# Performance work log

Measured on AMD Instinct MI355X. Metric: run time of the kernel, lower is better.

## Reference

```python
import jax, jax.numpy as jnp
import numpy as np

B = 16384
F = 26          # num categorical fields
V = 100000      # vocab per field (equal sizes)
N = 13          # num numeric fields
D = 32          # embed_dim
HIDDEN = [256, 128, 64]


def setup_inputs() -> dict:
    key = jax.random.key(0)
    ks = jax.random.split(key, 16)
    x_cat = jax.random.randint(ks[0], (B, F), 0, V)
    x_num = jax.random.normal(ks[1], (B, N), dtype=jnp.float32)
    # first-order and second-order embedding tables (all fields stacked)
    emb0 = jax.random.normal(ks[2], (F, V), dtype=jnp.float32) * 0.01      # linear weights per cat value
    emb1 = jax.random.normal(ks[3], (F, V, D), dtype=jnp.float32) * 0.01   # latent vectors per cat value
    num_bias = jnp.zeros((N,), dtype=jnp.float32)
    num_emb = jax.random.normal(ks[4], (N, D), dtype=jnp.float32) * 0.01
    # MLP params: input_dim = (F+N)*D -> 256 -> 128 -> 64
    dims = [(F + N) * D] + HIDDEN
    params = {}
    for i in range(len(HIDDEN)):
        fan_in = dims[i]
        bound = 1.0 / np.sqrt(fan_in)
        params[f"W{i+1}"] = jax.random.uniform(ks[5 + 2 * i], (fan_in, dims[i + 1]), minval=-bound, maxval=bound, dtype=jnp.float32)
        params[f"b{i+1}"] = jax.random.uniform(ks[6 + 2 * i], (dims[i + 1],), minval=-bound, maxval=bound, dtype=jnp.float32)
    head_in = HIDDEN[-1] + 2
    hb = 1.0 / np.sqrt(head_in)
    Wc = jax.random.uniform(ks[11], (head_in, 1), minval=-hb, maxval=hb, dtype=jnp.float32)
    bc = jax.random.uniform(ks[12], (1,), minval=-hb, maxval=hb, dtype=jnp.float32)
    Wo = jax.random.uniform(ks[13], (head_in, 1), minval=-hb, maxval=hb, dtype=jnp.float32)
    bo = jax.random.uniform(ks[14], (1,), minval=-hb, maxval=hb, dtype=jnp.float32)
    return {"x_cat": x_cat, "x_num": x_num, "emb0": emb0, "emb1": emb1,
            "num_bias": num_bias, "num_emb": num_emb,
            "W1": params["W1"], "b1": params["b1"],
            "W2": params["W2"], "b2": params["b2"],
            "W3": params["W3"], "b3": params["b3"],
            "Wc": Wc, "bc": bc, "Wo": Wo, "bo": bo}


def reference(x_cat, x_num, emb0, emb1, num_bias, num_emb,
              W1, b1, W2, b2, W3, b3, Wc, bc, Wo, bo):
    f_idx = jnp.arange(F)
    # ---- first-order (linear) term ----
    linear_cat = emb0[f_idx[None, :], x_cat]                 # [B, F]
    linear_num = x_num * num_bias[None, :]                   # [B, N]
    linear_term = (linear_cat.sum(axis=1) + linear_num.sum(axis=1))[:, None]  # [B, 1]
    # ---- embeddings for FM + deep ----
    cat_e = emb1[f_idx[None, :], x_cat]                      # [B, F, D] fused gather
    num_e = x_num[:, :, None] * num_emb[None, :, :]          # [B, N, D]
    all_emb = jnp.concatenate([cat_e, num_e], axis=1)        # [B, F+N, D]
    # ---- FM second-order: 0.5 * sum((sum v)^2 - sum v^2) ----
    sum_emb = all_emb.sum(axis=1)                            # [B, D]
    square_sum = (all_emb * all_emb).sum(axis=1)             # [B, D]
    fm_second = 0.5 * (sum_emb * sum_emb - square_sum).sum(axis=1, keepdims=True)  # [B, 1]
    # ---- deep MLP (dropout = identity in eval) ----
    h = all_emb.reshape(all_emb.shape[0], -1)                # [B, (F+N)*D]
    h = jax.nn.relu(h @ W1 + b1)
    h = jax.nn.relu(h @ W2 + b2)
    h = jax.nn.relu(h @ W3 + b3)
    concat = jnp.concatenate([h, linear_term, fm_second], axis=1)  # [B, 66]
    logit1 = concat @ Wc + bc
    logit2 = concat @ Wo + bo
    return logit1, logit2
```

## Files before the change

### kernel.cpp

```cpp
#include <hip/hip_runtime.h>
#include <stdint.h>

#define B_ROWS 16384
#define NF 26
#define NV 100000
#define NN 13
#define ND 32
#define K1DIM 1248
#define H1DIM 256
#define H2DIM 128
#define H3DIM 64

typedef float f32x4 __attribute__((ext_vector_type(4)));
typedef short bf16x8 __attribute__((ext_vector_type(8)));

static __device__ __forceinline__ unsigned short f2bf(float f) {
    unsigned int u = __float_as_uint(f);
    unsigned int r = (u + 0x7fffu + ((u >> 16) & 1u)) >> 16;
    return (unsigned short)r;
}

static __device__ __forceinline__ void store_bf4(unsigned short* p, f32x4 e) {
    uint2 u;
    u.x = (unsigned)f2bf(e.x) | ((unsigned)f2bf(e.y) << 16);
    u.y = (unsigned)f2bf(e.z) | ((unsigned)f2bf(e.w) << 16);
    *(uint2*)p = u;
}

#define S1P ((K1DIM/32)*H1DIM*32)
#define S2P ((H1DIM/32)*H2DIM*32)
#define S3P ((H2DIM/32)*H3DIM*32)
#define EMB_BLOCKS 512
#define RPK_BLOCKS ((S1P + S2P + S3P) / 256)

__global__ __launch_bounds__(256) void prep(
    const int* __restrict__ x_cat, const float* __restrict__ x_num,
    const float* __restrict__ emb0, const float* __restrict__ emb1,
    const float* __restrict__ num_bias, const float* __restrict__ num_emb,
    const float* __restrict__ W1, const float* __restrict__ W2, const float* __restrict__ W3,
    unsigned short* __restrict__ Xp, float* __restrict__ lin_out, float* __restrict__ fm_out,
    unsigned short* __restrict__ W1p, unsigned short* __restrict__ W2p, unsigned short* __restrict__ W3p)
{
    if (blockIdx.x >= EMB_BLOCKS) {
        int tid = (blockIdx.x - EMB_BLOCKS) * 256 + threadIdx.x;
        if (tid < S1P) {
            int kk = tid & 31; int n = (tid >> 5) & (H1DIM - 1); int kt = tid >> 13;
            W1p[tid] = f2bf(W1[(kt * 32 + kk) * H1DIM + n]);
        } else if (tid < S1P + S2P) {
            int t = tid - S1P;
            int kk = t & 31; int n = (t >> 5) & (H2DIM - 1); int kt = t >> 12;
            W2p[t] = f2bf(W2[(kt * 32 + kk) * H2DIM + n]);
        } else {
            int t = tid - S1P - S2P;
            int kk = t & 31; int n = (t >> 5) & (H3DIM - 1); int kt = t >> 11;
            W3p[t] = f2bf(W3[(kt * 32 + kk) * H3DIM + n]);
        }
        return;
    }

    int sub = threadIdx.x & 7;
    int row = blockIdx.x * 32 + (threadIdx.x >> 3);
    int lanebase = (threadIdx.x & 63) & 56;

    const int* xc = x_cat + row * NF;
    int idxh[4];
#pragma unroll
    for (int j = 0; j < 4; j++) { int f = sub + 8 * j; idxh[j] = (f < NF) ? xc[f] : 0; }
    float numh[2];
    numh[0] = x_num[row * NN + sub];
    numh[1] = (sub < NN - 8) ? x_num[row * NN + sub + 8] : 0.f;

    float lv = 0.f;
#pragma unroll
    for (int j = 0; j < 4; j++) { int f = sub + 8 * j; if (f < NF) lv += emb0[f * NV + idxh[j]]; }
    lv += numh[0] * num_bias[sub];
    if (sub < NN - 8) lv += numh[1] * num_bias[sub + 8];

    unsigned short* xr = Xp + (size_t)row * K1DIM;
    f32x4 s4 = (f32x4){0.f, 0.f, 0.f, 0.f};
    f32x4 q4 = (f32x4){0.f, 0.f, 0.f, 0.f};

#pragma unroll
    for (int f = 0; f < NF; ++f) {
        int idx = __shfl(idxh[f >> 3], lanebase + (f & 7), 64);
        f32x4 e = ((const f32x4*)(emb1 + (size_t)(f * NV + idx) * ND))[sub];
        s4 += e; q4 += e * e;
        store_bf4(xr + f * ND + sub * 4, e);
    }
#pragma unroll
    for (int n = 0; n < NN; ++n) {
        float xv = __shfl(numh[n >> 3], lanebase + (n & 7), 64);
        f32x4 w = ((const f32x4*)(num_emb + n * ND))[sub];
        f32x4 e = w * xv;
        s4 += e; q4 += e * e;
        store_bf4(xr + (NF + n) * ND + sub * 4, e);
    }

    float val = s4.x * s4.x + s4.y * s4.y + s4.z * s4.z + s4.w * s4.w
              - (q4.x + q4.y + q4.z + q4.w);
#pragma unroll
    for (int m = 1; m < 8; m <<= 1) {
        val += __shfl_xor(val, m, 64);
        lv  += __shfl_xor(lv,  m, 64);
    }
    if (sub == 0) { fm_out[row] = 0.5f * val; lin_out[row] = lv; }
}

template<int TMM, int TMN>
__global__ __launch_bounds__(256) void gemm_relu(
    const unsigned short* __restrict__ X, const unsigned short* __restrict__ Wp,
    const float* __restrict__ bias, unsigned short* __restrict__ Y,
    int M, int N, int K)
{
    int wave = blockIdx.x * 4 + (threadIdx.x >> 6);
    int lane = threadIdx.x & 63;
    int l15 = lane & 15, quad = lane >> 4;
    int nWaveN = N / (16 * TMN);
    int wm = wave / nWaveN, wn = wave % nWaveN;
    int m0 = wm * 16 * TMM, n0 = wn * 16 * TMN;

    f32x4 acc[TMM][TMN];
#pragma unroll
    for (int i = 0; i < TMM; i++)
#pragma unroll
        for (int j = 0; j < TMN; j++) acc[i][j] = (f32x4){0.f, 0.f, 0.f, 0.f};

    const unsigned short* aptr = X + (size_t)(m0 + l15) * K + quad * 8;
    const unsigned short* bptr = Wp + ((size_t)n0 + l15) * 32 + quad * 8;
    const int KT = K >> 5;

    bf16x8 a[TMM], b[TMN];
#pragma unroll
    for (int i = 0; i < TMM; i++) a[i] = *(const bf16x8*)(aptr + (size_t)i * 16 * K);
#pragma unroll
    for (int j = 0; j < TMN; j++) b[j] = *(const bf16x8*)(bptr + (size_t)j * 16 * 32);

    for (int kt = 0; kt < KT - 1; ++kt) {
        bf16x8 an[TMM], bn[TMN];
        const unsigned short* ap = aptr + (size_t)(kt + 1) * 32;
        const unsigned short* bp = bptr + (size_t)(kt + 1) * N * 32;
#pragma unroll
        for (int i = 0; i < TMM; i++) an[i] = *(const bf16x8*)(ap + (size_t)i * 16 * K);
#pragma unroll
        for (int j = 0; j < TMN; j++) bn[j] = *(const bf16x8*)(bp + (size_t)j * 16 * 32);
#pragma unroll
        for (int i = 0; i < TMM; i++)
#pragma unroll
            for (int j = 0; j < TMN; j++)
                acc[i][j] = __builtin_amdgcn_mfma_f32_16x16x32_bf16(a[i], b[j], acc[i][j], 0, 0, 0);
#pragma unroll
        for (int i = 0; i < TMM; i++) a[i] = an[i];
#pragma unroll
        for (int j = 0; j < TMN; j++) b[j] = bn[j];
    }
#pragma unroll
    for (int i = 0; i < TMM; i++)
#pragma unroll
        for (int j = 0; j < TMN; j++)
            acc[i][j] = __builtin_amdgcn_mfma_f32_16x16x32_bf16(a[i], b[j], acc[i][j], 0, 0, 0);

#pragma unroll
    for (int j = 0; j < TMN; j++) {
        int col = n0 + j * 16 + l15;
        float bv = bias[col];
#pragma unroll
        for (int i = 0; i < TMM; i++) {
            int rbase = m0 + i * 16 + quad * 4;
#pragma unroll
            for (int r = 0; r < 4; r++) {
                float v = acc[i][j][r] + bv;
                v = v > 0.f ? v : 0.f;
                Y[(size_t)(rbase + r) * N + col] = f2bf(v);
            }
        }
    }
}

#define LDP 136
__global__ __launch_bounds__(256) void gemm23_head(
    const unsigned short* __restrict__ H1, const unsigned short* __restrict__ W2p,
    const float* __restrict__ b2,
    const unsigned short* __restrict__ W3p, const float* __restrict__ b3,
    const float* __restrict__ Wc, const float* __restrict__ bc,
    const float* __restrict__ Wo, const float* __restrict__ bo,
    const float* __restrict__ lin, const float* __restrict__ fm,
    float* __restrict__ out)
{
    __shared__ unsigned short lds[4 * 16 * LDP];
    int wid  = threadIdx.x >> 6;
    int wave = blockIdx.x * 4 + wid;
    int lane = threadIdx.x & 63;
    int l15 = lane & 15, quad = lane >> 4;
    int m0 = wave * 16;
    unsigned short* wlds = lds + wid * 16 * LDP;

    f32x4 acc2[8];
#pragma unroll
    for (int j = 0; j < 8; j++) acc2[j] = (f32x4){0.f, 0.f, 0.f, 0.f};

    const unsigned short* aptr = H1 + (size_t)(m0 + l15) * H1DIM + quad * 8;
    const unsigned short* bptr = W2p + l15 * 32 + quad * 8;
#pragma unroll
    for (int kt = 0; kt < 8; ++kt) {
        bf16x8 a = *(const bf16x8*)(aptr + kt * 32);
#pragma unroll
        for (int j = 0; j < 8; j++) {
            bf16x8 b = *(const bf16x8*)(bptr + (kt * H2DIM + j * 16) * 32);
            acc2[j] = __builtin_amdgcn_mfma_f32_16x16x32_bf16(a, b, acc2[j], 0, 0, 0);
        }
    }
#pragma unroll
    for (int j = 0; j < 8; j++) {
        int col = j * 16 + l15;
        float bv = b2[col];
#pragma unroll
        for (int r = 0; r < 4; r++) {
            float v = acc2[j][r] + bv;
            v = v > 0.f ? v : 0.f;
            wlds[(quad * 4 + r) * LDP + col] = f2bf(v);
        }
    }
    __syncthreads();

    f32x4 acc3[4];
#pragma unroll
    for (int j = 0; j < 4; j++) acc3[j] = (f32x4){0.f, 0.f, 0.f, 0.f};

    const unsigned short* b3ptr = W3p + l15 * 32 + quad * 8;
#pragma unroll
    for (int kt = 0; kt < 4; ++kt) {
        bf16x8 a = *(const bf16x8*)(wlds + l15 * LDP + kt * 32 + quad * 8);
#pragma unroll
        for (int j = 0; j < 4; j++) {
            bf16x8 b = *(const bf16x8*)(b3ptr + (kt * H3DIM + j * 16) * 32);
            acc3[j] = __builtin_amdgcn_mfma_f32_16x16x32_bf16(a, b, acc3[j], 0, 0, 0);
        }
    }

    float s1r[4] = {0.f, 0.f, 0.f, 0.f};
    float s2r[4] = {0.f, 0.f, 0.f, 0.f};
#pragma unroll
    for (int j = 0; j < 4; j++) {
        int col = j * 16 + l15;
        float bv = b3[col], wc = Wc[col], wo = Wo[col];
#pragma unroll
        for (int r = 0; r < 4; r++) {
            float v = acc3[j][r] + bv;
            v = v > 0.f ? v : 0.f;
            s1r[r] += v * wc;
            s2r[r] += v * wo;
        }
    }
#pragma unroll
    for (int r = 0; r < 4; r++) {
#pragma unroll
        for (int m = 8; m >= 1; m >>= 1) {
            s1r[r] += __shfl_xor(s1r[r], m, 16);
            s2r[r] += __shfl_xor(s2r[r], m, 16);
        }
    }
    if (l15 == 0) {
        float wc64 = Wc[64], wc65 = Wc[65], wo64 = Wo[64], wo65 = Wo[65];
        float bcv = bc[0], bov = bo[0];
#pragma unroll
        for (int r = 0; r < 4; r++) {
            int row = m0 + quad * 4 + r;
            float lt = lin[row], f2 = fm[row];
            out[row]          = s1r[r] + lt * wc64 + f2 * wc65 + bcv;
            out[B_ROWS + row] = s2r[r] + lt * wo64 + f2 * wo65 + bov;
        }
    }
}

#define OFF_XP   ((size_t)0)
#define OFF_W1P  ((size_t)40894464)
#define OFF_W2P  (OFF_W1P + 638976)
#define OFF_W3P  (OFF_W2P + 65536)
#define OFF_H1   (OFF_W3P + 16384)
#define OFF_LIN  (OFF_H1 + 8388608)
#define OFF_FM   (OFF_LIN + 65536)

extern "C" void kernel_launch(void* const* d_in, const int* in_sizes, int n_in,
                              void* d_out, int out_size, void* d_ws, size_t ws_size,
                              hipStream_t stream)
{
    const int*   x_cat    = (const int*)d_in[0];
    const float* x_num    = (const float*)d_in[1];
    const float* emb0     = (const float*)d_in[2];
    const float* emb1     = (const float*)d_in[3];
    const float* num_bias = (const float*)d_in[4];
    const float* num_emb  = (const float*)d_in[5];
    const float* W1 = (const float*)d_in[6];
    const float* b1 = (const float*)d_in[7];
    const float* W2 = (const float*)d_in[8];
    const float* b2 = (const float*)d_in[9];
    const float* W3 = (const float*)d_in[10];
    const float* b3 = (const float*)d_in[11];
    const float* Wc = (const float*)d_in[12];
    const float* bc = (const float*)d_in[13];
    const float* Wo = (const float*)d_in[14];
    const float* bo = (const float*)d_in[15];
    float* out = (float*)d_out;

    char* ws = (char*)d_ws;
    unsigned short* Xp  = (unsigned short*)(ws + OFF_XP);
    unsigned short* W1p = (unsigned short*)(ws + OFF_W1P);
    unsigned short* W2p = (unsigned short*)(ws + OFF_W2P);
    unsigned short* W3p = (unsigned short*)(ws + OFF_W3P);
    unsigned short* H1  = (unsigned short*)(ws + OFF_H1);
    float* lin = (float*)(ws + OFF_LIN);
    float* fm  = (float*)(ws + OFF_FM);

    prep<<<EMB_BLOCKS + RPK_BLOCKS, 256, 0, stream>>>(
        x_cat, x_num, emb0, emb1, num_bias, num_emb, W1, W2, W3,
        Xp, lin, fm, W1p, W2p, W3p);
    gemm_relu<2, 2><<<1024, 256, 0, stream>>>(Xp, W1p, b1, H1, B_ROWS, H1DIM, K1DIM);
    gemm23_head<<<B_ROWS / 16 / 4, 256, 0, stream>>>(H1, W2p, b2, W3p, b3, Wc, bc, Wo, bo, lin, fm, out);
}
```

Measured before the change: 466.6 us.

## Fuse embedding gather, three MLP layers and head into one LDS-resident kernel

Replaces the separate embedding/prep, layer-1 GEMM and layer-2/3/head kernels with one fused kernel. Each 32-row block gathers its embeddings straight into shared memory, then runs all three GEMMs and the heads from LDS. Weight repacking moves to its own small kernel. This removes the global round-trip of the 40MB bf16 activation matrix and the H1 buffer, at the cost of large LDS use (about 80KB per block), which limits occupancy. Every block also re-streams all of W1 from cache, with only 512 blocks of 32 rows each.

```diff
diff --git a/kernel.cpp b/kernel.cpp
--- a/kernel.cpp
+++ b/kernel.cpp
@@ -11,6 +11,11 @@
 #define H2DIM 128
 #define H3DIM 64
 
+#define XSTR  1256
+#define H1STR 264
+#define H2STR 136
+#define H2OFF (32 * H1STR)
+
 typedef float f32x4 __attribute__((ext_vector_type(4)));
 typedef short bf16x8 __attribute__((ext_vector_type(8)));
 
@@ -20,265 +25,257 @@
     return (unsigned short)r;
 }
 
-static __device__ __forceinline__ void store_bf4(unsigned short* p, f32x4 e) {
+static __device__ __forceinline__ uint2 pack_bf4(f32x4 e) {
     uint2 u;
     u.x = (unsigned)f2bf(e.x) | ((unsigned)f2bf(e.y) << 16);
     u.y = (unsigned)f2bf(e.z) | ((unsigned)f2bf(e.w) << 16);
-    *(uint2*)p = u;
+    return u;
 }
 
 #define S1P ((K1DIM/32)*H1DIM*32)
 #define S2P ((H1DIM/32)*H2DIM*32)
 #define S3P ((H2DIM/32)*H3DIM*32)
-#define EMB_BLOCKS 512
-#define RPK_BLOCKS ((S1P + S2P + S3P) / 256)
-
-__global__ __launch_bounds__(256) void prep(
+
+__global__ __launch_bounds__(256) void repack_weights(
+    const float* __restrict__ W1, const float* __restrict__ W2, const float* __restrict__ W3,
+    unsigned short* __restrict__ W1p, unsigned short* __restrict__ W2p, unsigned short* __restrict__ W3p)
+{
+    int tid = blockIdx.x * 256 + threadIdx.x;
+    if (tid < S1P) {
+        int kk = tid & 31; int n = (tid >> 5) & (H1DIM - 1); int kt = tid >> 13;
+        W1p[tid] = f2bf(W1[(kt * 32 + kk) * H1DIM + n]);
+    } else if (tid < S1P + S2P) {
+        int t = tid - S1P;
+        int kk = t & 31; int n = (t >> 5) & (H2DIM - 1); int kt = t >> 12;
+        W2p[t] = f2bf(W2[(kt * 32 + kk) * H2DIM + n]);
+    } else if (tid < S1P + S2P + S3P) {
+        int t = tid - S1P - S2P;
+        int kk = t & 31; int n = (t >> 5) & (H3DIM - 1); int kt = t >> 11;
+        W3p[t] = f2bf(W3[(kt * 32 + kk) * H3DIM + n]);
+    }
+}
+
+__global__ __launch_bounds__(256, 2) void deepfm_fused(
     const int* __restrict__ x_cat, const float* __restrict__ x_num,
     const float* __restrict__ emb0, const float* __restrict__ emb1,
     const float* __restrict__ num_bias, const float* __restrict__ num_emb,
-    const float* __restrict__ W1, const float* __restrict__ W2, const float* __restrict__ W3,
-    unsigned short* __restrict__ Xp, float* __restrict__ lin_out, float* __restrict__ fm_out,
-    unsigned short* __restrict__ W1p, unsigned short* __restrict__ W2p, unsigned short* __restrict__ W3p)
-{
-    if (blockIdx.x >= EMB_BLOCKS) {
-        int tid = (blockIdx.x - EMB_BLOCKS) * 256 + threadIdx.x;
-        if (tid < S1P) {
-            int kk = tid & 31; int n = (tid >> 5) & (H1DIM - 1); int kt = tid >> 13;
-            W1p[tid] = f2bf(W1[(kt * 32 + kk) * H1DIM + n]);
-        } else if (tid < S1P + S2P) {
-            int t = tid - S1P;
-            int kk = t & 31; int n = (t >> 5) & (H2DIM - 1); int kt = t >> 12;
-            W2p[t] = f2bf(W2[(kt * 32 + kk) * H2DIM + n]);
-        } else {
-            int t = tid - S1P - S2P;
-            int kk = t & 31; int n = (t >> 5) & (H3DIM - 1); int kt = t >> 11;
-            W3p[t] = f2bf(W3[(kt * 32 + kk) * H3DIM + n]);
-        }
-        return;
-    }
-
-    int sub = threadIdx.x & 7;
-    int row = blockIdx.x * 32 + (threadIdx.x >> 3);
-    int lanebase = (threadIdx.x & 63) & 56;
-
-    const int* xc = x_cat + row * NF;
-    int idxh[4];
-#pragma unroll
-    for (int j = 0; j < 4; j++) { int f = sub + 8 * j; idxh[j] = (f < NF) ? xc[f] : 0; }
-    float numh[2];
-    numh[0] = x_num[row * NN + sub];
-    numh[1] = (sub < NN - 8) ? x_num[row * NN + sub + 8] : 0.f;
-
-    float lv = 0.f;
-#pragma unroll
-    for (int j = 0; j < 4; j++) { int f = sub + 8 * j; if (f < NF) lv += emb0[f * NV + idxh[j]]; }
-    lv += numh[0] * num_bias[sub];
-    if (sub < NN - 8) lv += numh[1] * num_bias[sub + 8];
-
-    unsigned short* xr = Xp + (size_t)row * K1DIM;
-    f32x4 s4 = (f32x4){0.f, 0.f, 0.f, 0.f};
-    f32x4 q4 = (f32x4){0.f, 0.f, 0.f, 0.f};
-
-#pragma unroll
-    for (int f = 0; f < NF; ++f) {
-        int idx = __shfl(idxh[f >> 3], lanebase + (f & 7), 64);
-        f32x4 e = ((const f32x4*)(emb1 + (size_t)(f * NV + idx) * ND))[sub];
-        s4 += e; q4 += e * e;
-        store_bf4(xr + f * ND + sub * 4, e);
-    }
-#pragma unroll
-    for (int n = 0; n < NN; ++n) {
-        float xv = __shfl(numh[n >> 3], lanebase + (n & 7), 64);
-        f32x4 w = ((const f32x4*)(num_emb + n * ND))[sub];
-        f32x4 e = w * xv;
-        s4 += e; q4 += e * e;
-        store_bf4(xr + (NF + n) * ND + sub * 4, e);
-    }
-
-    float val = s4.x * s4.x + s4.y * s4.y + s4.z * s4.z + s4.w * s4.w
-              - (q4.x + q4.y + q4.z + q4.w);
-#pragma unroll
-    for (int m = 1; m < 8; m <<= 1) {
-        val += __shfl_xor(val, m, 64);
-        lv  += __shfl_xor(lv,  m, 64);
-    }
-    if (sub == 0) { fm_out[row] = 0.5f * val; lin_out[row] = lv; }
-}
-
-template<int TMM, int TMN>
-__global__ __launch_bounds__(256) void gemm_relu(
-    const unsigned short* __restrict__ X, const unsigned short* __restrict__ Wp,
-    const float* __restrict__ bias, unsigned short* __restrict__ Y,
-    int M, int N, int K)
-{
-    int wave = blockIdx.x * 4 + (threadIdx.x >> 6);
-    int lane = threadIdx.x & 63;
-    int l15 = lane & 15, quad = lane >> 4;
-    int nWaveN = N / (16 * TMN);
-    int wm = wave / nWaveN, wn = wave % nWaveN;
-    int m0 = wm * 16 * TMM, n0 = wn * 16 * TMN;
-
-    f32x4 acc[TMM][TMN];
-#pragma unroll
-    for (int i = 0; i < TMM; i++)
-#pragma unroll
-        for (int j = 0; j < TMN; j++) acc[i][j] = (f32x4){0.f, 0.f, 0.f, 0.f};
-
-    const unsigned short* aptr = X + (size_t)(m0 + l15) * K + quad * 8;
-    const unsigned short* bptr = Wp + ((size_t)n0 + l15) * 32 + quad * 8;
-    const int KT = K >> 5;
-
-    bf16x8 a[TMM], b[TMN];
-#pragma unroll
-    for (int i = 0; i < TMM; i++) a[i] = *(const bf16x8*)(aptr + (size_t)i * 16 * K);
-#pragma unroll
-    for (int j = 0; j < TMN; j++) b[j] = *(const bf16x8*)(bptr + (size_t)j * 16 * 32);
-
-    for (int kt = 0; kt < KT - 1; ++kt) {
-        bf16x8 an[TMM], bn[TMN];
-        const unsigned short* ap = aptr + (size_t)(kt + 1) * 32;
-        const unsigned short* bp = bptr + (size_t)(kt + 1) * N * 32;
-#pragma unroll
-        for (int i = 0; i < TMM; i++) an[i] = *(const bf16x8*)(ap + (size_t)i * 16 * K);
-#pragma unroll
-        for (int j = 0; j < TMN; j++) bn[j] = *(const bf16x8*)(bp + (size_t)j * 16 * 32);
-#pragma unroll
-        for (int i = 0; i < TMM; i++)
-#pragma unroll
-            for (int j = 0; j < TMN; j++)
-                acc[i][j] = __builtin_amdgcn_mfma_f32_16x16x32_bf16(a[i], b[j], acc[i][j], 0, 0, 0);
-#pragma unroll
-        for (int i = 0; i < TMM; i++) a[i] = an[i];
-#pragma unroll
-        for (int j = 0; j < TMN; j++) b[j] = bn[j];
-    }
-#pragma unroll
-    for (int i = 0; i < TMM; i++)
-#pragma unroll
-        for (int j = 0; j < TMN; j++)
-            acc[i][j] = __builtin_amdgcn_mfma_f32_16x16x32_bf16(a[i], b[j], acc[i][j], 0, 0, 0);
-
-#pragma unroll
-    for (int j = 0; j < TMN; j++) {
-        int col = n0 + j * 16 + l15;
-        float bv = bias[col];
-#pragma unroll
-        for (int i = 0; i < TMM; i++) {
-            int rbase = m0 + i * 16 + quad * 4;
-#pragma unroll
-            for (int r = 0; r < 4; r++) {
-                float v = acc[i][j][r] + bv;
-                v = v > 0.f ? v : 0.f;
-                Y[(size_t)(rbase + r) * N + col] = f2bf(v);
-            }
-        }
-    }
-}
-
-#define LDP 136
-__global__ __launch_bounds__(256) void gemm23_head(
-    const unsigned short* __restrict__ H1, const unsigned short* __restrict__ W2p,
-    const float* __restrict__ b2,
+    const unsigned short* __restrict__ W1p, const float* __restrict__ b1,
+    const unsigned short* __restrict__ W2p, const float* __restrict__ b2,
     const unsigned short* __restrict__ W3p, const float* __restrict__ b3,
     const float* __restrict__ Wc, const float* __restrict__ bc,
     const float* __restrict__ Wo, const float* __restrict__ bo,
-    const float* __restrict__ lin, const float* __restrict__ fm,
     float* __restrict__ out)
 {
-    __shared__ unsigned short lds[4 * 16 * LDP];
-    int wid  = threadIdx.x >> 6;
-    int wave = blockIdx.x * 4 + wid;
-    int lane = threadIdx.x & 63;
-    int l15 = lane & 15, quad = lane >> 4;
-    int m0 = wave * 16;
-    unsigned short* wlds = lds + wid * 16 * LDP;
-
-    f32x4 acc2[8];
-#pragma unroll
-    for (int j = 0; j < 8; j++) acc2[j] = (f32x4){0.f, 0.f, 0.f, 0.f};
-
-    const unsigned short* aptr = H1 + (size_t)(m0 + l15) * H1DIM + quad * 8;
-    const unsigned short* bptr = W2p + l15 * 32 + quad * 8;
-#pragma unroll
-    for (int kt = 0; kt < 8; ++kt) {
-        bf16x8 a = *(const bf16x8*)(aptr + kt * 32);
-#pragma unroll
-        for (int j = 0; j < 8; j++) {
-            bf16x8 b = *(const bf16x8*)(bptr + (kt * H2DIM + j * 16) * 32);
-            acc2[j] = __builtin_amdgcn_mfma_f32_16x16x32_bf16(a, b, acc2[j], 0, 0, 0);
-        }
-    }
-#pragma unroll
-    for (int j = 0; j < 8; j++) {
-        int col = j * 16 + l15;
+    __shared__ unsigned short Xs[32 * XSTR];
+    __shared__ float s_fm[32], s_lin[32];
+
+    const int tid  = threadIdx.x;
+    const int wid  = tid >> 6;
+    const int lane = tid & 63;
+    const int l15  = lane & 15, quad = lane >> 4;
+    const int row0 = blockIdx.x * 32;
+
+    {
+        int sub  = tid & 7;
+        int rowL = tid >> 3;
+        int row  = row0 + rowL;
+        int lanebase = lane & 56;
+
+        const int* xc = x_cat + row * NF;
+        int idxh[4];
+#pragma unroll
+        for (int j = 0; j < 4; j++) { int f = sub + 8 * j; idxh[j] = (f < NF) ? xc[f] : 0; }
+        float numh0 = x_num[row * NN + sub];
+        float numh1 = (sub < NN - 8) ? x_num[row * NN + sub + 8] : 0.f;
+
+        float lv = 0.f;
+#pragma unroll
+        for (int j = 0; j < 4; j++) { int f = sub + 8 * j; if (f < NF) lv += emb0[f * NV + idxh[j]]; }
+        lv += numh0 * num_bias[sub];
+        if (sub < NN - 8) lv += numh1 * num_bias[sub + 8];
+
+        unsigned short* xr = &Xs[rowL * XSTR];
+        f32x4 s4 = (f32x4){0.f, 0.f, 0.f, 0.f};
+        f32x4 q4 = (f32x4){0.f, 0.f, 0.f, 0.f};
+#pragma unroll
+        for (int f = 0; f < NF; ++f) {
+            int idx = __shfl(idxh[f >> 3], lanebase + (f & 7), 64);
+            f32x4 e = ((const f32x4*)(emb1 + (size_t)(f * NV + idx) * ND))[sub];
+            s4 += e; q4 += e * e;
+            *(uint2*)(xr + f * ND + sub * 4) = pack_bf4(e);
+        }
+#pragma unroll
+        for (int n = 0; n < NN; ++n) {
+            float xv = __shfl((n < 8) ? numh0 : numh1, lanebase + (n & 7), 64);
+            f32x4 w = ((const f32x4*)(num_emb + n * ND))[sub];
+            f32x4 e = w * xv;
+            s4 += e; q4 += e * e;
+            *(uint2*)(xr + (NF + n) * ND + sub * 4) = pack_bf4(e);
+        }
+        float val = s4.x * s4.x + s4.y * s4.y + s4.z * s4.z + s4.w * s4.w
+                  - (q4.x + q4.y + q4.z + q4.w);
+#pragma unroll
+        for (int m = 1; m < 8; m <<= 1) {
+            val += __shfl_xor(val, m, 64);
+            lv  += __shfl_xor(lv,  m, 64);
+        }
+        if (sub == 0) { s_fm[rowL] = 0.5f * val; s_lin[rowL] = lv; }
+    }
+    __syncthreads();
+
+    f32x4 acc1[2][4];
+#pragma unroll
+    for (int i = 0; i < 2; i++)
+#pragma unroll
+        for (int j = 0; j < 4; j++) acc1[i][j] = (f32x4){0.f, 0.f, 0.f, 0.f};
+
+    {
+        const unsigned short* bptr = W1p + ((size_t)(wid * 64) + l15) * 32 + quad * 8;
+        const unsigned short* abase = &Xs[l15 * XSTR + quad * 8];
+        const int KT = K1DIM / 32;
+
+        bf16x8 a[2], b[4];
+#pragma unroll
+        for (int i = 0; i < 2; i++) a[i] = *(const bf16x8*)(abase + i * 16 * XSTR);
+#pragma unroll
+        for (int j = 0; j < 4; j++) b[j] = *(const bf16x8*)(bptr + j * 512);
+
+        for (int kt = 0; kt < KT - 1; ++kt) {
+            bf16x8 an[2], bn[4];
+            const unsigned short* ap = abase + (kt + 1) * 32;
+            const unsigned short* bp = bptr + (size_t)(kt + 1) * (H1DIM * 32);
+#pragma unroll
+            for (int i = 0; i < 2; i++) an[i] = *(const bf16x8*)(ap + i * 16 * XSTR);
+#pragma unroll
+            for (int j = 0; j < 4; j++) bn[j] = *(const bf16x8*)(bp + j * 512);
+#pragma unroll
+            for (int i = 0; i < 2; i++)
+#pragma unroll
+                for (int j = 0; j < 4; j++)
+                    acc1[i][j] = __builtin_amdgcn_mfma_f32_16x16x32_bf16(a[i], b[j], acc1[i][j], 0, 0, 0);
+#pragma unroll
+            for (int i = 0; i < 2; i++) a[i] = an[i];
+#pragma unroll
+            for (int j = 0; j < 4; j++) b[j] = bn[j];
+        }
+#pragma unroll
+        for (int i = 0; i < 2; i++)
+#pragma unroll
+            for (int j = 0; j < 4; j++)
+                acc1[i][j] = __builtin_amdgcn_mfma_f32_16x16x32_bf16(a[i], b[j], acc1[i][j], 0, 0, 0);
+    }
+    __syncthreads();
+
+#pragma unroll
+    for (int j = 0; j < 4; j++) {
+        int col = wid * 64 + j * 16 + l15;
+        float bv = b1[col];
+#pragma unroll
+        for (int i = 0; i < 2; i++) {
+#pragma unroll
+            for (int r = 0; r < 4; r++) {
+                float v = acc1[i][j][r] + bv;
+                v = v > 0.f ? v : 0.f;
+                Xs[(i * 16 + quad * 4 + r) * H1STR + col] = f2bf(v);
+            }
+        }
+    }
+    __syncthreads();
+
+    f32x4 acc2[2][2];
+#pragma unroll
+    for (int i = 0; i < 2; i++)
+#pragma unroll
+        for (int j = 0; j < 2; j++) acc2[i][j] = (f32x4){0.f, 0.f, 0.f, 0.f};
+    {
+        const unsigned short* bptr = W2p + ((size_t)(wid * 32) + l15) * 32 + quad * 8;
+        const unsigned short* abase = &Xs[l15 * H1STR + quad * 8];
+#pragma unroll
+        for (int kt = 0; kt < 8; ++kt) {
+            bf16x8 a[2], b[2];
+#pragma unroll
+            for (int i = 0; i < 2; i++) a[i] = *(const bf16x8*)(abase + i * 16 * H1STR + kt * 32);
+#pragma unroll
+            for (int j = 0; j < 2; j++) b[j] = *(const bf16x8*)(bptr + (size_t)kt * (H2DIM * 32) + j * 512);
+#pragma unroll
+            for (int i = 0; i < 2; i++)
+#pragma unroll
+                for (int j = 0; j < 2; j++)
+                    acc2[i][j] = __builtin_amdgcn_mfma_f32_16x16x32_bf16(a[i], b[j], acc2[i][j], 0, 0, 0);
+        }
+    }
+#pragma unroll
+    for (int j = 0; j < 2; j++) {
+        int col = wid * 32 + j * 16 + l15;
         float bv = b2[col];
 #pragma unroll
+        for (int i = 0; i < 2; i++) {
+#pragma unroll
+            for (int r = 0; r < 4; r++) {
+                float v = acc2[i][j][r] + bv;
+                v = v > 0.f ? v : 0.f;
+                Xs[H2OFF + (i * 16 + quad * 4 + r) * H2STR + col] = f2bf(v);
+            }
+        }
+    }
+    __syncthreads();
+
+    if (wid < 2) {
+        int m0l = wid * 16;
+        f32x4 acc3[4];
+#pragma unroll
+        for (int j = 0; j < 4; j++) acc3[j] = (f32x4){0.f, 0.f, 0.f, 0.f};
+        const unsigned short* abase = &Xs[H2OFF + (m0l + l15) * H2STR + quad * 8];
+        const unsigned short* bptr = W3p + (size_t)l15 * 32 + quad * 8;
+#pragma unroll
+        for (int kt = 0; kt < 4; ++kt) {
+            bf16x8 a = *(const bf16x8*)(abase + kt * 32);
+#pragma unroll
+            for (int j = 0; j < 4; j++) {
+                bf16x8 b = *(const bf16x8*)(bptr + (kt * H3DIM + j * 16) * 32);
+                acc3[j] = __builtin_amdgcn_mfma_f32_16x16x32_bf16(a, b, acc3[j], 0, 0, 0);
+            }
+        }
+        float s1r[4] = {0.f, 0.f, 0.f, 0.f};
+        float s2r[4] = {0.f, 0.f, 0.f, 0.f};
+#pragma unroll
+        for (int j = 0; j < 4; j++) {
+            int col = j * 16 + l15;
+            float bv = b3[col], wc = Wc[col], wo = Wo[col];
+#pragma unroll
+            for (int r = 0; r < 4; r++) {
+                float v = acc3[j][r] + bv;
+                v = v > 0.f ? v : 0.f;
+                s1r[r] += v * wc;
+                s2r[r] += v * wo;
+            }
+        }
+#pragma unroll
         for (int r = 0; r < 4; r++) {
-            float v = acc2[j][r] + bv;
-            v = v > 0.f ? v : 0.f;
-            wlds[(quad * 4 + r) * LDP + col] = f2bf(v);
-        }
-    }
-    __syncthreads();
-
-    f32x4 acc3[4];
-#pragma unroll
-    for (int j = 0; j < 4; j++) acc3[j] = (f32x4){0.f, 0.f, 0.f, 0.f};
-
-    const unsigned short* b3ptr = W3p + l15 * 32 + quad * 8;
-#pragma unroll
-    for (int kt = 0; kt < 4; ++kt) {
-        bf16x8 a = *(const bf16x8*)(wlds + l15 * LDP + kt * 32 + quad * 8);
-#pragma unroll
-        for (int j = 0; j < 4; j++) {
-            bf16x8 b = *(const bf16x8*)(b3ptr + (kt * H3DIM + j * 16) * 32);
-            acc3[j] = __builtin_amdgcn_mfma_f32_16x16x32_bf16(a, b, acc3[j], 0, 0, 0);
-        }
-    }
-
-    float s1r[4] = {0.f, 0.f, 0.f, 0.f};
-    float s2r[4] = {0.f, 0.f, 0.f, 0.f};
-#pragma unroll
-    for (int j = 0; j < 4; j++) {
-        int col = j * 16 + l15;
-        float bv = b3[col], wc = Wc[col], wo = Wo[col];
-#pragma unroll
-        for (int r = 0; r < 4; r++) {
-            float v = acc3[j][r] + bv;
-            v = v > 0.f ? v : 0.f;
-            s1r[r] += v * wc;
-            s2r[r] += v * wo;
-        }
-    }
-#pragma unroll
-    for (int r = 0; r < 4; r++) {
-#pragma unroll
-        for (int m = 8; m >= 1; m >>= 1) {
-            s1r[r] += __shfl_xor(s1r[r], m, 16);
-            s2r[r] += __shfl_xor(s2r[r], m, 16);
-        }
-    }
-    if (l15 == 0) {
-        float wc64 = Wc[64], wc65 = Wc[65], wo64 = Wo[64], wo65 = Wo[65];
-        float bcv = bc[0], bov = bo[0];
-#pragma unroll
-        for (int r = 0; r < 4; r++) {
-            int row = m0 + quad * 4 + r;
-            float lt = lin[row], f2 = fm[row];
-            out[row]          = s1r[r] + lt * wc64 + f2 * wc65 + bcv;
-            out[B_ROWS + row] = s2r[r] + lt * wo64 + f2 * wo65 + bov;
-        }
-    }
-}
-
-#define OFF_XP   ((size_t)0)
-#define OFF_W1P  ((size_t)40894464)
-#define OFF_W2P  (OFF_W1P + 638976)
-#define OFF_W3P  (OFF_W2P + 65536)
-#define OFF_H1   (OFF_W3P + 16384)
-#define OFF_LIN  (OFF_H1 + 8388608)
-#define OFF_FM   (OFF_LIN + 65536)
+#pragma unroll
+            for (int m = 8; m >= 1; m >>= 1) {
+                s1r[r] += __shfl_xor(s1r[r], m, 16);
+                s2r[r] += __shfl_xor(s2r[r], m, 16);
+            }
+        }
+        if (l15 == 0) {
+            float wc64 = Wc[64], wc65 = Wc[65], wo64 = Wo[64], wo65 = Wo[65];
+            float bcv = bc[0], bov = bo[0];
+#pragma unroll
+            for (int r = 0; r < 4; r++) {
+                int rl = m0l + quad * 4 + r;
+                int row = row0 + rl;
+                float lt = s_lin[rl], f2 = s_fm[rl];
+                out[row]          = s1r[r] + lt * wc64 + f2 * wc65 + bcv;
+                out[B_ROWS + row] = s2r[r] + lt * wo64 + f2 * wo65 + bov;
+            }
+        }
+    }
+}
+
+#define OFF_W1P  ((size_t)0)
+#define OFF_W2P  (OFF_W1P + (size_t)S1P * 2)
+#define OFF_W3P  (OFF_W2P + (size_t)S2P * 2)
 
 extern "C" void kernel_launch(void* const* d_in, const int* in_sizes, int n_in,
                               void* d_out, int out_size, void* d_ws, size_t ws_size,
@@ -303,17 +300,12 @@
     float* out = (float*)d_out;
 
     char* ws = (char*)d_ws;
-    unsigned short* Xp  = (unsigned short*)(ws + OFF_XP);
     unsigned short* W1p = (unsigned short*)(ws + OFF_W1P);
     unsigned short* W2p = (unsigned short*)(ws + OFF_W2P);
     unsigned short* W3p = (unsigned short*)(ws + OFF_W3P);
-    unsigned short* H1  = (unsigned short*)(ws + OFF_H1);
-    float* lin = (float*)(ws + OFF_LIN);
-    float* fm  = (float*)(ws + OFF_FM);
-
-    prep<<<EMB_BLOCKS + RPK_BLOCKS, 256, 0, stream>>>(
-        x_cat, x_num, emb0, emb1, num_bias, num_emb, W1, W2, W3,
-        Xp, lin, fm, W1p, W2p, W3p);
-    gemm_relu<2, 2><<<1024, 256, 0, stream>>>(Xp, W1p, b1, H1, B_ROWS, H1DIM, K1DIM);
-    gemm23_head<<<B_ROWS / 16 / 4, 256, 0, stream>>>(H1, W2p, b2, W3p, b3, Wc, bc, Wo, bo, lin, fm, out);
-}
+
+    repack_weights<<<(S1P + S2P + S3P) / 256, 256, 0, stream>>>(W1, W2, W3, W1p, W2p, W3p);
+    deepfm_fused<<<B_ROWS / 32, 256, 0, stream>>>(
+        x_cat, x_num, emb0, emb1, num_bias, num_emb,
+        W1p, b1, W2p, b2, W3p, b3, Wc, bc, Wo, bo, out);
+}
```

New measurement: 435.9 us. 6.6% less time.
